# Performance work log

Hardware: AMD Instinct MI355X
Metric: run time of the kernel (lower is better)

## Reference

```python
import jax, jax.numpy as jnp
import numpy as np

B, S, D, H, DFF = 8, 1024, 1024, 16, 4096
DK = D // H
EPS = 1e-5


def setup_inputs() -> dict:
    key = jax.random.key(0)
    ks = jax.random.split(key, 12)
    sc = lambda n: 1.0 / np.sqrt(n)
    return {
        "x": jax.random.normal(ks[0], (B, S, D), jnp.float32),
        "src_mask": jnp.ones((B, 1, 1, S), jnp.int32),
        "wq": jax.random.normal(ks[1], (D, D), jnp.float32) * sc(D),
        "bq": jnp.zeros((D,), jnp.float32),
        "wk": jax.random.normal(ks[2], (D, D), jnp.float32) * sc(D),
        "bk": jnp.zeros((D,), jnp.float32),
        "wv": jax.random.normal(ks[3], (D, D), jnp.float32) * sc(D),
        "bv": jnp.zeros((D,), jnp.float32),
        "wo": jax.random.normal(ks[4], (D, D), jnp.float32) * sc(D),
        "bo": jnp.zeros((D,), jnp.float32),
        "w1": jax.random.normal(ks[5], (DFF, D), jnp.float32) * sc(D),
        "b1": jnp.zeros((DFF,), jnp.float32),
        "w2": jax.random.normal(ks[6], (D, DFF), jnp.float32) * sc(DFF),
        "b2": jnp.zeros((D,), jnp.float32),
        "g1": jnp.ones((1,), jnp.float32),
        "be1": jnp.zeros((1,), jnp.float32),
        "g2": jnp.ones((1,), jnp.float32),
        "be2": jnp.zeros((1,), jnp.float32),
    }


def _layernorm(x, gamma, beta):
    # Faithful to source: torch.var defaults to unbiased (ddof=1); scalar gamma/beta.
    mu = jnp.mean(x, axis=-1, keepdims=True)
    var = jnp.var(x, axis=-1, keepdims=True, ddof=1)
    return gamma * (x - mu) / jnp.sqrt(var + EPS) + beta


def _mha(x, wq, bq, wk, bk, wv, bv, wo, bo):
    q = (x @ wq.T + bq).reshape(B, S, H, DK).transpose(0, 2, 1, 3)
    k = (x @ wk.T + bk).reshape(B, S, H, DK).transpose(0, 2, 1, 3)
    v = (x @ wv.T + bv).reshape(B, S, H, DK).transpose(0, 2, 1, 3)
    scores = jnp.einsum("bhqd,bhkd->bhqk", q, k) / np.sqrt(DK)
    # NOTE: source uses non-inplace masked_fill whose result is discarded,
    # so the mask has no effect on the executed math; we replicate that.
    attn = jax.nn.softmax(scores, axis=-1)
    out = jnp.einsum("bhqk,bhkd->bhqd", attn, v)
    out = out.transpose(0, 2, 1, 3).reshape(B, S, D)
    return out @ wo.T + bo


def reference(x, src_mask, wq, bq, wk, bk, wv, bv, wo, bo,
              w1, b1, w2, b2, g1, be1, g2, be2):
    # residual 1: pre-norm self-attention (dropout=0 in eval)
    x = x + _mha(_layernorm(x, g1, be1), wq, bq, wk, bk, wv, bv, wo, bo)
    # residual 2: pre-norm FFN
    h = _layernorm(x, g2, be2)
    ff = jax.nn.relu(h @ w1.T + b1) @ w2.T + b2
    return x + ff
```

## Files before the change

kernel.cpp:

```cpp
#include <hip/hip_runtime.h>

typedef unsigned short u16;
typedef unsigned int u32;
typedef __attribute__((ext_vector_type(8))) __bf16 bf16x8;
typedef __attribute__((ext_vector_type(4))) float f32x4;

#define B_ 8
#define S_ 1024
#define D_ 1024
#define H_ 16
#define DK_ 64
#define DFF_ 4096
#define LDQKV 3072

__device__ __forceinline__ float bflo(u32 u) { return __uint_as_float(u << 16); }
__device__ __forceinline__ float bfhi(u32 u) { return __uint_as_float(u & 0xffff0000u); }
__device__ __forceinline__ u16 f2bf(float f) {
    u32 u = __float_as_uint(f);
    u += 0x7fffu + ((u >> 16) & 1u);
    return (u16)(u >> 16);
}
__device__ __forceinline__ u32 cvtpk(float lo, float hi) {
    u32 r;
    asm("v_cvt_pk_bf16_f32 %0, %1, %2" : "=v"(r) : "v"(lo), "v"(hi));
    return r;
}

__device__ __forceinline__ void gl2lds16(const u16* g, u16* l) {
    __builtin_amdgcn_global_load_lds(
        (const __attribute__((address_space(1))) void*)g,
        (__attribute__((address_space(3))) void*)l, 16, 0, 0);
}

__global__ __launch_bounds__(256) void sniff_kernel(const u16* __restrict__ w,
                                                    int* __restrict__ flag) {
    float mx = 0.f;
    for (int i = threadIdx.x; i < 4096; i += 256) {
        float v = fabsf(bflo((u32)w[i]));
        if (!isnan(v)) mx = fmaxf(mx, v);
    }
#pragma unroll
    for (int m = 1; m < 64; m <<= 1) mx = fmaxf(mx, __shfl_xor(mx, m, 64));
    __shared__ float wmx[4];
    if ((threadIdx.x & 63) == 0) wmx[threadIdx.x >> 6] = mx;
    __syncthreads();
    if (threadIdx.x == 0) {
        float m2 = fmaxf(fmaxf(wmx[0], wmx[1]), fmaxf(wmx[2], wmx[3]));
        *flag = (m2 > 1e3f) ? 1 : 0;
    }
}

__global__ __launch_bounds__(256) void norm_kernel(const void* __restrict__ in,
                                                   u16* __restrict__ out, int n,
                                                   const int* __restrict__ flag) {
    const int i = blockIdx.x * 256 + threadIdx.x;
    if (i >= n) return;
    if (*flag)
        out[i] = f2bf(((const float*)in)[i]);
    else
        out[i] = ((const u16*)in)[i];
}

struct SmallTbl {
    const void* src[10];
    u16* dst[10];
    int n[10];
};
__global__ __launch_bounds__(256) void norm_small(SmallTbl tb,
                                                  const int* __restrict__ flag) {
    int i = blockIdx.x * 256 + threadIdx.x;
    const int f = *flag;
#pragma unroll
    for (int j = 0; j < 10; ++j) {
        if (i < tb.n[j]) {
            if (f)
                tb.dst[j][i] = f2bf(((const float*)tb.src[j])[i]);
            else
                tb.dst[j][i] = ((const u16*)tb.src[j])[i];
            return;
        }
        i -= tb.n[j];
    }
}

template <int INF>
__global__ __launch_bounds__(256) void ln_kernel(const void* __restrict__ in,
                                                 const u16* __restrict__ gs,
                                                 const u16* __restrict__ bs,
                                                 u16* __restrict__ out,
                                                 const int* __restrict__ flag) {
    const int row = blockIdx.x, t = threadIdx.x;
    const bool f32in = (INF == 1) || (INF == 2 && flag[0] != 0);
    float v0, v1, v2, v3;
    if (f32in) {
        const float* p = (const float*)in + (size_t)row * D_ + t * 4;
        float4 f = *(const float4*)p;
        v0 = f.x; v1 = f.y; v2 = f.z; v3 = f.w;
    } else {
        const u16* p = (const u16*)in + (size_t)row * D_ + t * 4;
        uint2 u = *(const uint2*)p;
        v0 = bflo(u.x); v1 = bfhi(u.x); v2 = bflo(u.y); v3 = bfhi(u.y);
    }
    float s = v0 + v1 + v2 + v3;
    float sq = v0 * v0 + v1 * v1 + v2 * v2 + v3 * v3;
#pragma unroll
    for (int m = 1; m < 64; m <<= 1) {
        s += __shfl_xor(s, m, 64);
        sq += __shfl_xor(sq, m, 64);
    }
    __shared__ float ss[4], sqs[4];
    const int w = t >> 6;
    if ((t & 63) == 0) { ss[w] = s; sqs[w] = sq; }
    __syncthreads();
    s = ss[0] + ss[1] + ss[2] + ss[3];
    sq = sqs[0] + sqs[1] + sqs[2] + sqs[3];
    const float mu = s * (1.f / 1024.f);
    float var = (sq - 1024.f * mu * mu) * (1.f / 1023.f);
    var = fmaxf(var, 0.f);
    const float rstd = rsqrtf(var + 1e-5f);
    const float gm = bflo((u32)gs[0]);
    const float bt = bflo((u32)bs[0]);
    const float y0 = gm * (v0 - mu) * rstd + bt;
    const float y1 = gm * (v1 - mu) * rstd + bt;
    const float y2 = gm * (v2 - mu) * rstd + bt;
    const float y3 = gm * (v3 - mu) * rstd + bt;
    uint2 uo;
    uo.x = (u32)f2bf(y0) | ((u32)f2bf(y1) << 16);
    uo.y = (u32)f2bf(y2) | ((u32)f2bf(y3) << 16);
    *(uint2*)(out + (size_t)row * D_ + t * 4) = uo;
}

template <int RELU, int RES, int OUTF>
__global__ __launch_bounds__(256, 4) void gemm_bt(const u16* __restrict__ A,
                                                  const u16* __restrict__ W,
                                                  const u16* __restrict__ bias,
                                                  const void* __restrict__ res,
                                                  void* __restrict__ out,
                                                  int M, int N, int K,
                                                  const int* __restrict__ oflag) {
    __shared__ __align__(16) u16 As[128 * 64];
    __shared__ __align__(16) u16 Bs[128 * 64];
    const int t = threadIdx.x;
    const int lane = t & 63, w = t >> 6;
    const int wm = w >> 1, wn = w & 1;

    const int nx = N >> 7;
    const int gsz = nx << 3;
    const int id = blockIdx.x;
    const int grp = id / gsz;
    const int rem = id - grp * gsz;
    const int m0 = ((grp << 3) + (rem & 7)) << 7;
    const int n0 = (rem >> 3) << 7;

    f32x4 acc[4][4];
#pragma unroll
    for (int mi = 0; mi < 4; ++mi)
#pragma unroll
        for (int ni = 0; ni < 4; ++ni) acc[mi][ni] = (f32x4){0.f, 0.f, 0.f, 0.f};

    const int r8 = lane >> 3, s8 = lane & 7;
    const int cg = s8 ^ r8;
    const u16* Ag = A + (size_t)(m0 + w * 8 + r8) * K + cg * 8;
    const u16* Bg = W + (size_t)(n0 + w * 8 + r8) * K + cg * 8;
    const size_t rI = (size_t)32 * K;
    u16* Asd = &As[(w * 8) * 64];
    u16* Bsd = &Bs[(w * 8) * 64];

    const int c = lane & 15, g = lane >> 4;
    const u16* As_r = &As[(wm * 64 + c) * 64];
    const u16* Bs_r = &Bs[(wn * 64 + c) * 64];
    const int sl0 = (g ^ (c & 7)) * 8;
    const int sl1 = ((4 + g) ^ (c & 7)) * 8;

    for (int kt = 0; kt < K; kt += 64) {
        __syncthreads();
        gl2lds16(Ag, Asd);
        gl2lds16(Ag + rI, Asd + 32 * 64);
        gl2lds16(Ag + 2 * rI, Asd + 64 * 64);
        gl2lds16(Ag + 3 * rI, Asd + 96 * 64);
        gl2lds16(Bg, Bsd);
        gl2lds16(Bg + rI, Bsd + 32 * 64);
        gl2lds16(Bg + 2 * rI, Bsd + 64 * 64);
        gl2lds16(Bg + 3 * rI, Bsd + 96 * 64);
        Ag += 64; Bg += 64;
        __syncthreads();
#pragma unroll
        for (int kc = 0; kc < 2; ++kc) {
            const int sl = kc ? sl1 : sl0;
            bf16x8 af[4], bfr[4];
#pragma unroll
            for (int i = 0; i < 4; ++i) {
                af[i] = *(const bf16x8*)(As_r + i * 16 * 64 + sl);
                bfr[i] = *(const bf16x8*)(Bs_r + i * 16 * 64 + sl);
            }
#pragma unroll
            for (int mi = 0; mi < 4; ++mi)
#pragma unroll
                for (int ni = 0; ni < 4; ++ni)
                    acc[mi][ni] = __builtin_amdgcn_mfma_f32_16x16x32_bf16(af[mi], bfr[ni], acc[mi][ni], 0, 0, 0);
        }
    }

    const int fl = oflag ? oflag[0] : 0;
    const bool f32o = (OUTF == 1) || (OUTF == 2 && fl != 0);
    const int qd = lane >> 4, cl = lane & 15;
#pragma unroll
    for (int ni = 0; ni < 4; ++ni) {
        const int col = n0 + wn * 64 + ni * 16 + cl;
        const float bv = bflo((u32)bias[col]);
#pragma unroll
        for (int mi = 0; mi < 4; ++mi) {
#pragma unroll
            for (int j = 0; j < 4; ++j) {
                const int row = m0 + wm * 64 + mi * 16 + qd * 4 + j;
                float vv = acc[mi][ni][j] + bv;
                if (RELU) vv = fmaxf(vv, 0.f);
                if (RES == 2) vv += ((const float*)res)[(size_t)row * N + col];
                if (RES == 3) {
                    if (fl)
                        vv += ((const float*)res)[(size_t)row * N + col];
                    else
                        vv += bflo((u32)((const u16*)res)[(size_t)row * N + col]);
                }
                if (f32o)
                    ((float*)out)[(size_t)row * N + col] = vv;
                else
                    ((u16*)out)[(size_t)row * N + col] = f2bf(vv);
            }
        }
    }
}

template <int RELU>
__global__ __launch_bounds__(512, 2) void gemm256(const u16* __restrict__ A,
                                                  const u16* __restrict__ W,
                                                  const u16* __restrict__ bias,
                                                  u16* __restrict__ out,
                                                  int M, int N, int K) {
    __shared__ __align__(16) u16 As[2][2][256 * 32];
    __shared__ __align__(16) u16 Bs[2][2][256 * 32];
    const int t = threadIdx.x;
    const int lane = t & 63, w = t >> 6;
    const int wm = w >> 2, wn = w & 3;

    const int nx = N >> 8;
    const int gsz = nx << 3;
    const int id = blockIdx.x;
    const int grp = id / gsz;
    const int rem = id - grp * gsz;
    const int m0 = ((grp << 3) + (rem & 7)) << 8;
    const int n0 = (rem >> 3) << 8;

    f32x4 acc[8][4];
#pragma unroll
    for (int mi = 0; mi < 8; ++mi)
#pragma unroll
        for (int ni = 0; ni < 4; ++ni) acc[mi][ni] = (f32x4){0.f, 0.f, 0.f, 0.f};

    const int vr = lane >> 2, vs = lane & 3;
    const int cgs = vs ^ ((vr >> 1) & 3);
    const u16* Asrc = A + (size_t)(m0 + w * 16 + vr) * K + cgs * 8;
    const u16* Bsrc = W + (size_t)(n0 + w * 16 + vr) * K + cgs * 8;
    const size_t rI = (size_t)128 * K;

    auto stageA = [&](int p, int kc, int tk) {
        u16* d = &As[p][kc][(w * 16) * 32];
        const u16* s = Asrc + (size_t)tk * 64 + kc * 32;
        gl2lds16(s, d);
        gl2lds16(s + rI, d + 128 * 32);
    };
    auto stageB = [&](int p, int kc, int tk) {
        u16* d = &Bs[p][kc][(w * 16) * 32];
        const u16* s = Bsrc + (size_t)tk * 64 + kc * 32;
        gl2lds16(s, d);
        gl2lds16(s + rI, d + 128 * 32);
    };

    const int c = lane & 15, g = lane >> 4;
    const int sx = (g ^ ((c >> 1) & 3)) << 3;

    const int nt = K >> 6;
    stageA(0, 0, 0); stageB(0, 0, 0);
    stageA(0, 1, 0); stageB(0, 1, 0);
    stageA(1, 0, 1); stageB(1, 0, 1);
    asm volatile("s_waitcnt vmcnt(4)" ::: "memory");
    __builtin_amdgcn_s_barrier();
    __builtin_amdgcn_sched_barrier(0);

    int cur = 0;
    for (int kt = 0; kt < nt; ++kt) {
#pragma unroll
        for (int ph = 0; ph < 4; ++ph) {
            const int kc = ph >> 1, qm = ph & 1;
            bf16x8 af[4], bfv[4];
            const u16* Ab = &As[cur][kc][0];
            const u16* Bb = &Bs[cur][kc][0];
#pragma unroll
            for (int i = 0; i < 4; ++i)
                af[i] = *(const bf16x8*)(Ab + (wm * 128 + (qm * 4 + i) * 16 + c) * 32 + sx);
#pragma unroll
            for (int i = 0; i < 4; ++i)
                bfv[i] = *(const bf16x8*)(Bb + (wn * 64 + i * 16 + c) * 32 + sx);
            if (ph == 0) { if (kt + 1 < nt) stageA(cur ^ 1, 1, kt + 1); }
            else if (ph == 1) { if (kt + 1 < nt) stageB(cur ^ 1, 1, kt + 1); }
            else if (ph == 2) { if (kt + 2 < nt) stageA(cur, 0, kt + 2); }
            else { if (kt + 2 < nt) stageB(cur, 0, kt + 2); }
            __builtin_amdgcn_s_barrier();
            __builtin_amdgcn_s_setprio(1);
#pragma unroll
            for (int mi = 0; mi < 4; ++mi)
#pragma unroll
                for (int ni = 0; ni < 4; ++ni)
                    acc[qm * 4 + mi][ni] = __builtin_amdgcn_mfma_f32_16x16x32_bf16(
                        af[mi], bfv[ni], acc[qm * 4 + mi][ni], 0, 0, 0);
            __builtin_amdgcn_s_setprio(0);
            if (ph < 3) {
                __builtin_amdgcn_s_barrier();
                if (ph == 1) __builtin_amdgcn_sched_barrier(0);
            }
        }
        if (kt < nt - 2)
            asm volatile("s_waitcnt vmcnt(4)" ::: "memory");
        else
            asm volatile("s_waitcnt vmcnt(0)" ::: "memory");
        __builtin_amdgcn_s_barrier();
        __builtin_amdgcn_sched_barrier(0);
        cur ^= 1;
    }

#pragma unroll
    for (int mi = 0; mi < 8; ++mi) {
#pragma unroll
        for (int j = 0; j < 4; ++j) {
            const int row = m0 + wm * 128 + mi * 16 + g * 4 + j;
#pragma unroll
            for (int ni = 0; ni < 4; ++ni) {
                const int col = n0 + wn * 64 + ni * 16 + c;
                float vv = acc[mi][ni][j] + bflo((u32)bias[col]);
                if (RELU) vv = fmaxf(vv, 0.f);
                out[(size_t)row * N + col] = f2bf(vv);
            }
        }
    }
}

__global__ __launch_bounds__(256, 2) void attn_mfma(const u16* __restrict__ QKV,
                                                    u16* __restrict__ O) {
    __shared__ __align__(16) u16 lds[6 * 64 * 64];
    u16* Ks = lds;
    u16* VsT = lds + 64 * 64;

    const int t = threadIdx.x;
    const int lane = t & 63, w = t >> 6;
    u16* Pw = lds + (2 + w) * 64 * 64;
    const int b = blockIdx.y >> 4, h = blockIdx.y & 15;
    const int q_base = blockIdx.x * 256 + w * 64;
    const int c = lane & 15, g = lane >> 4;
    const int c7 = c & 7;
    const float SC = 0.18033688011112042f;

    bf16x8 qfrag[4][2];
#pragma unroll
    for (int ni = 0; ni < 4; ++ni)
#pragma unroll
        for (int kc = 0; kc < 2; ++kc)
            qfrag[ni][kc] = *(const bf16x8*)(QKV + (size_t)(b * S_ + q_base + 16 * ni + c) * LDQKV +
                                             h * 64 + kc * 32 + 8 * g);

    f32x4 acc_o[4][4];
#pragma unroll
    for (int mi = 0; mi < 4; ++mi)
#pragma unroll
        for (int ni = 0; ni < 4; ++ni) acc_o[mi][ni] = (f32x4){0.f, 0.f, 0.f, 0.f};
    float m_st[4] = {-1e30f, -1e30f, -1e30f, -1e30f};
    float l_st[4] = {0.f, 0.f, 0.f, 0.f};

    const size_t kbase = (size_t)(b * S_) * LDQKV + 1024 + h * 64;
    const size_t vbase = (size_t)(b * S_) * LDQKV + 2048 + h * 64;

    const int r8 = lane >> 3, s8 = lane & 7;
    const int cgk = s8 ^ r8;
    const u16* Kg = QKV + kbase + (size_t)(w * 8 + r8) * LDQKV + cgk * 8;
    u16* Ksd = &Ks[(w * 8) * 64];
    const size_t rIk = (size_t)32 * LDQKV;

    const int vr = t >> 3, vdq = t & 7;
    const u16* Vg = QKV + vbase + (size_t)(2 * vr) * LDQKV + vdq * 8;

    int vfx[4];
#pragma unroll
    for (int mi = 0; mi < 4; ++mi) vfx[mi] = c7 ^ ((2 * mi + (c >> 3)) & 7);

    for (int kt = 0; kt < 16; ++kt) {
        __syncthreads();
        gl2lds16(Kg, Ksd);
        gl2lds16(Kg + rIk, Ksd + 32 * 64);
        Kg += (size_t)64 * LDQKV;
        {
            uint4 a = *(const uint4*)Vg;
            uint4 bb = *(const uint4*)(Vg + LDQKV);
            Vg += (size_t)64 * LDQKV;
            const u32 aw[4] = {a.x, a.y, a.z, a.w};
            const u32 bw[4] = {bb.x, bb.y, bb.z, bb.w};
#pragma unroll
            for (int i = 0; i < 8; ++i) {
                u32 wv;
                if (i & 1)
                    wv = (aw[i >> 1] >> 16) | (bw[i >> 1] & 0xffff0000u);
                else
                    wv = (aw[i >> 1] & 0xffffu) | (bw[i >> 1] << 16);
                const int d = vdq * 8 + i;
                *(u32*)&VsT[d * 64 + (((vr >> 2) ^ (i ^ vdq)) << 3) + ((vr & 3) << 1)] = wv;
            }
        }
        __syncthreads();

        f32x4 acc_s[4][4];
#pragma unroll
        for (int mi = 0; mi < 4; ++mi)
#pragma unroll
            for (int ni = 0; ni < 4; ++ni) acc_s[mi][ni] = (f32x4){0.f, 0.f, 0.f, 0.f};
        __builtin_amdgcn_s_setprio(1);
#pragma unroll
        for (int kc = 0; kc < 2; ++kc) {
            bf16x8 kf[4];
#pragma unroll
            for (int mi = 0; mi < 4; ++mi)
                kf[mi] = *(const bf16x8*)&Ks[(16 * mi + c) * 64 + (((kc * 4 + g) ^ c7) << 3)];
#pragma unroll
            for (int mi = 0; mi < 4; ++mi)
#pragma unroll
                for (int ni = 0; ni < 4; ++ni)
                    acc_s[mi][ni] = __builtin_amdgcn_mfma_f32_16x16x32_bf16(
                        kf[mi], qfrag[ni][kc], acc_s[mi][ni], 0, 0, 0);
        }
        __builtin_amdgcn_s_setprio(0);

        float alpha[4];
        bool resc[4];
#pragma unroll
        for (int ni = 0; ni < 4; ++ni) {
            float mx = -1e30f;
#pragma unroll
            for (int mi = 0; mi < 4; ++mi) {
#pragma unroll
                for (int j = 0; j < 4; ++j) mx = fmaxf(mx, acc_s[mi][ni][j]);
            }
            mx = fmaxf(mx, __shfl_xor(mx, 16, 64));
            mx = fmaxf(mx, __shfl_xor(mx, 32, 64));
            const float mo = m_st[ni];
            const float mn = fmaxf(mo, mx);
            resc[ni] = __any(mn > mo);
            if (resc[ni]) {
                alpha[ni] = exp2f((mo - mn) * SC);
                m_st[ni] = mn;
            } else {
                alpha[ni] = 1.f;
            }
            const float nms = m_st[ni] * SC;
            float sum = 0.f;
#pragma unroll
            for (int mi = 0; mi < 4; ++mi) {
                const float p0 = exp2f(fmaf(acc_s[mi][ni][0], SC, -nms));
                const float p1 = exp2f(fmaf(acc_s[mi][ni][1], SC, -nms));
                const float p2 = exp2f(fmaf(acc_s[mi][ni][2], SC, -nms));
                const float p3 = exp2f(fmaf(acc_s[mi][ni][3], SC, -nms));
                sum += (p0 + p1) + (p2 + p3);
                uint2 pk;
                pk.x = cvtpk(p0, p1);
                pk.y = cvtpk(p2, p3);
                *(uint2*)&Pw[(16 * ni + c) * 64 +
                             ((((2 * mi + (g >> 1)) ^ c7) << 3) + ((g & 1) << 2))] = pk;
            }
            sum += __shfl_xor(sum, 16, 64);
            sum += __shfl_xor(sum, 32, 64);
            l_st[ni] = (resc[ni] ? l_st[ni] * alpha[ni] : l_st[ni]) + sum;
        }
#pragma unroll
        for (int ni = 0; ni < 4; ++ni) {
            if (resc[ni]) {
#pragma unroll
                for (int mi = 0; mi < 4; ++mi) {
#pragma unroll
                    for (int j = 0; j < 4; ++j) acc_o[mi][ni][j] *= alpha[ni];
                }
            }
        }

        __builtin_amdgcn_s_setprio(1);
#pragma unroll
        for (int kc = 0; kc < 2; ++kc) {
            bf16x8 vf[4], pf[4];
#pragma unroll
            for (int mi = 0; mi < 4; ++mi)
                vf[mi] = *(const bf16x8*)&VsT[(16 * mi + c) * 64 + (((kc * 4 + g) ^ vfx[mi]) << 3)];
#pragma unroll
            for (int ni = 0; ni < 4; ++ni)
                pf[ni] = *(const bf16x8*)&Pw[(16 * ni + c) * 64 + (((kc * 4 + g) ^ c7) << 3)];
#pragma unroll
            for (int mi = 0; mi < 4; ++mi)
#pragma unroll
                for (int ni = 0; ni < 4; ++ni)
                    acc_o[mi][ni] = __builtin_amdgcn_mfma_f32_16x16x32_bf16(
                        vf[mi], pf[ni], acc_o[mi][ni], 0, 0, 0);
        }
        __builtin_amdgcn_s_setprio(0);
    }

#pragma unroll
    for (int ni = 0; ni < 4; ++ni) {
        const float inv_l = 1.f / l_st[ni];
        u16* op = O + (size_t)(b * S_ + q_base + 16 * ni + c) * D_ + h * 64;
#pragma unroll
        for (int mi = 0; mi < 4; ++mi) {
            uint2 uo;
            uo.x = cvtpk(acc_o[mi][ni][0] * inv_l, acc_o[mi][ni][1] * inv_l);
            uo.y = cvtpk(acc_o[mi][ni][2] * inv_l, acc_o[mi][ni][3] * inv_l);
            *(uint2*)(op + 16 * mi + 4 * g) = uo;
        }
    }
}

extern "C" void kernel_launch(void* const* d_in, const int* in_sizes, int n_in,
                              void* d_out, int out_size, void* d_ws, size_t ws_size,
                              hipStream_t stream) {
    (void)in_sizes; (void)n_in; (void)out_size; (void)ws_size;
    char* ws = (char*)d_ws;
    const size_t MB = 1ull << 20;
    const size_t KB = 1024;
    u16* wqkv = (u16*)(ws + 16 * MB);
    u16* won  = (u16*)(ws + 22 * MB);
    u16* w1n  = (u16*)(ws + 24 * MB);
    u16* w2n  = (u16*)(ws + 32 * MB);
    u16* bqkv = (u16*)(ws + 40 * MB);
    u16* bon  = (u16*)(ws + 40 * MB + 64 * KB);
    u16* b1n  = (u16*)(ws + 40 * MB + 128 * KB);
    u16* b2n  = (u16*)(ws + 40 * MB + 192 * KB);
    u16* g1n  = (u16*)(ws + 40 * MB + 256 * KB);
    u16* be1n = (u16*)(ws + 40 * MB + 320 * KB);
    u16* g2n  = (u16*)(ws + 40 * MB + 384 * KB);
    u16* be2n = (u16*)(ws + 40 * MB + 448 * KB);
    int* flag = (int*)(ws + 40 * MB + 512 * KB);
    u16* h1   = (u16*)(ws + 48 * MB);
    u16* qkv  = (u16*)(ws + 64 * MB);
    float* x2 = (float*)(ws + 64 * MB);
    u16* h2   = (u16*)(ws + 96 * MB);
    u16* f1   = (u16*)(ws + 112 * MB);

    const int M = B_ * S_;

    sniff_kernel<<<1, 256, 0, stream>>>((const u16*)d_in[2], flag);
    auto nrm = [&](const void* in, u16* out, int n) {
        norm_kernel<<<(n + 255) / 256, 256, 0, stream>>>(in, out, n, flag);
    };
    nrm(d_in[2],  wqkv,               D_ * D_);
    nrm(d_in[4],  wqkv + D_ * D_,     D_ * D_);
    nrm(d_in[6],  wqkv + 2 * D_ * D_, D_ * D_);
    nrm(d_in[8],  won, D_ * D_);
    nrm(d_in[10], w1n, DFF_ * D_);
    nrm(d_in[12], w2n, D_ * DFF_);
    {
        SmallTbl tb;
        tb.src[0] = d_in[3];  tb.dst[0] = bqkv;          tb.n[0] = D_;
        tb.src[1] = d_in[5];  tb.dst[1] = bqkv + D_;     tb.n[1] = D_;
        tb.src[2] = d_in[7];  tb.dst[2] = bqkv + 2 * D_; tb.n[2] = D_;
        tb.src[3] = d_in[9];  tb.dst[3] = bon;           tb.n[3] = D_;
        tb.src[4] = d_in[11]; tb.dst[4] = b1n;           tb.n[4] = DFF_;
        tb.src[5] = d_in[13]; tb.dst[5] = b2n;           tb.n[5] = D_;
        tb.src[6] = d_in[14]; tb.dst[6] = g1n;           tb.n[6] = 1;
        tb.src[7] = d_in[15]; tb.dst[7] = be1n;          tb.n[7] = 1;
        tb.src[8] = d_in[16]; tb.dst[8] = g2n;           tb.n[8] = 1;
        tb.src[9] = d_in[17]; tb.dst[9] = be2n;          tb.n[9] = 1;
        const int tot = 5 * D_ + DFF_ + 4;
        norm_small<<<(tot + 255) / 256, 256, 0, stream>>>(tb, flag);
    }

    ln_kernel<2><<<M, 256, 0, stream>>>(d_in[0], g1n, be1n, h1, flag);
    gemm256<0><<<(LDQKV / 256) * (M / 256), 512, 0, stream>>>(h1, wqkv, bqkv, qkv, M, LDQKV, D_);
    attn_mfma<<<dim3(S_ / 256, B_ * H_), 256, 0, stream>>>(qkv, h1);
    gemm_bt<0, 3, 1><<<(D_ / 128) * (M / 128), 256, 0, stream>>>(h1, won, bon, d_in[0], x2, M, D_, D_, flag);
    ln_kernel<1><<<M, 256, 0, stream>>>((const void*)x2, g2n, be2n, h2, flag);
    gemm256<1><<<(DFF_ / 256) * (M / 256), 512, 0, stream>>>(h2, w1n, b1n, f1, M, DFF_, D_);
    gemm_bt<0, 2, 2><<<(D_ / 128) * (M / 128), 256, 0, stream>>>(f1, w2n, b2n, (const void*)x2, (void*)d_out, M, D_, DFF_, flag);
}
```

Baseline: 531.4 us.

## Add 128x256 eight-wave GEMM for output projection and FFN down-projection

Adds gemm_bn, a 512-thread GEMM with a 128x256 output tile, double-buffered direct global-to-LDS staging split across four phases, and swizzled LDS reads. It replaces the 128x128 gemm_bt kernels used for the attention output projection and the FFN second layer, with grouped block ordering for L2 reuse. The larger tile raises arithmetic intensity per block and overlaps loads with MFMA. The trade-off is half as many blocks for N=1024, which may reduce occupancy or balance across CUs.

```diff
diff --git a/kernel.cpp b/kernel.cpp
--- a/kernel.cpp
+++ b/kernel.cpp
@@ -339,6 +339,131 @@
                 float vv = acc[mi][ni][j] + bflo((u32)bias[col]);
                 if (RELU) vv = fmaxf(vv, 0.f);
                 out[(size_t)row * N + col] = f2bf(vv);
+            }
+        }
+    }
+}
+
+template <int RELU, int RES, int OUTF>
+__global__ __launch_bounds__(512, 2) void gemm_bn(const u16* __restrict__ A,
+                                                  const u16* __restrict__ W,
+                                                  const u16* __restrict__ bias,
+                                                  const void* __restrict__ res,
+                                                  void* __restrict__ out,
+                                                  int M, int N, int K,
+                                                  const int* __restrict__ oflag) {
+    __shared__ __align__(16) u16 As[2][2][128 * 32];
+    __shared__ __align__(16) u16 Bs[2][2][256 * 32];
+    const int t = threadIdx.x;
+    const int lane = t & 63, w = t >> 6;
+    const int wm = w >> 2, wn = w & 3;
+
+    const int nx = N >> 8;
+    const int gsz = nx << 3;
+    const int id = blockIdx.x;
+    const int grp = id / gsz;
+    const int rem = id - grp * gsz;
+    const int m0 = ((grp << 3) + (rem & 7)) << 7;
+    const int n0 = (rem >> 3) << 8;
+
+    f32x4 acc[4][4];
+#pragma unroll
+    for (int mi = 0; mi < 4; ++mi)
+#pragma unroll
+        for (int ni = 0; ni < 4; ++ni) acc[mi][ni] = (f32x4){0.f, 0.f, 0.f, 0.f};
+
+    const int vr = lane >> 2, vs = lane & 3;
+    const int cgs = vs ^ ((vr >> 1) & 3);
+    const u16* Asrc = A + (size_t)(m0 + w * 16 + vr) * K + cgs * 8;
+    const u16* Bsrc = W + (size_t)(n0 + w * 16 + vr) * K + cgs * 8;
+    const size_t rI = (size_t)128 * K;
+
+    auto stageA = [&](int p, int kc, int tk) {
+        u16* d = &As[p][kc][(w * 16) * 32];
+        gl2lds16(Asrc + (size_t)tk * 64 + kc * 32, d);
+    };
+    auto stageB = [&](int p, int kc, int tk) {
+        u16* d = &Bs[p][kc][(w * 16) * 32];
+        const u16* s = Bsrc + (size_t)tk * 64 + kc * 32;
+        gl2lds16(s, d);
+        gl2lds16(s + rI, d + 128 * 32);
+    };
+
+    const int c = lane & 15, g = lane >> 4;
+    const int sx = (g ^ ((c >> 1) & 3)) << 3;
+
+    const int nt = K >> 6;
+    stageA(0, 0, 0); stageB(0, 0, 0);
+    stageA(0, 1, 0); stageB(0, 1, 0);
+    stageA(1, 0, 1); stageB(1, 0, 1);
+    asm volatile("s_waitcnt vmcnt(3)" ::: "memory");
+    __builtin_amdgcn_s_barrier();
+    __builtin_amdgcn_sched_barrier(0);
+
+    int cur = 0;
+    for (int kt = 0; kt < nt; ++kt) {
+#pragma unroll
+        for (int ph = 0; ph < 4; ++ph) {
+            const int kc = ph >> 1, qm = ph & 1;
+            bf16x8 af[2], bfv[4];
+            const u16* Ab = &As[cur][kc][0];
+            const u16* Bb = &Bs[cur][kc][0];
+#pragma unroll
+            for (int i = 0; i < 2; ++i)
+                af[i] = *(const bf16x8*)(Ab + (wm * 64 + (qm * 2 + i) * 16 + c) * 32 + sx);
+#pragma unroll
+            for (int i = 0; i < 4; ++i)
+                bfv[i] = *(const bf16x8*)(Bb + (wn * 64 + i * 16 + c) * 32 + sx);
+            if (ph == 0) { if (kt + 1 < nt) stageA(cur ^ 1, 1, kt + 1); }
+            else if (ph == 1) { if (kt + 1 < nt) stageB(cur ^ 1, 1, kt + 1); }
+            else if (ph == 2) { if (kt + 2 < nt) stageA(cur, 0, kt + 2); }
+            else { if (kt + 2 < nt) stageB(cur, 0, kt + 2); }
+            __builtin_amdgcn_s_barrier();
+            __builtin_amdgcn_s_setprio(1);
+#pragma unroll
+            for (int mi = 0; mi < 2; ++mi)
+#pragma unroll
+                for (int ni = 0; ni < 4; ++ni)
+                    acc[qm * 2 + mi][ni] = __builtin_amdgcn_mfma_f32_16x16x32_bf16(
+                        af[mi], bfv[ni], acc[qm * 2 + mi][ni], 0, 0, 0);
+            __builtin_amdgcn_s_setprio(0);
+            if (ph < 3) {
+                __builtin_amdgcn_s_barrier();
+                if (ph == 1) __builtin_amdgcn_sched_barrier(0);
+            }
+        }
+        if (kt < nt - 2)
+            asm volatile("s_waitcnt vmcnt(3)" ::: "memory");
+        else
+            asm volatile("s_waitcnt vmcnt(0)" ::: "memory");
+        __builtin_amdgcn_s_barrier();
+        __builtin_amdgcn_sched_barrier(0);
+        cur ^= 1;
+    }
+
+    const int fl = oflag ? oflag[0] : 0;
+    const bool f32o = (OUTF == 1) || (OUTF == 2 && fl != 0);
+#pragma unroll
+    for (int mi = 0; mi < 4; ++mi) {
+#pragma unroll
+        for (int j = 0; j < 4; ++j) {
+            const int row = m0 + wm * 64 + mi * 16 + g * 4 + j;
+#pragma unroll
+            for (int ni = 0; ni < 4; ++ni) {
+                const int col = n0 + wn * 64 + ni * 16 + c;
+                float vv = acc[mi][ni][j] + bflo((u32)bias[col]);
+                if (RELU) vv = fmaxf(vv, 0.f);
+                if (RES == 2) vv += ((const float*)res)[(size_t)row * N + col];
+                if (RES == 3) {
+                    if (fl)
+                        vv += ((const float*)res)[(size_t)row * N + col];
+                    else
+                        vv += bflo((u32)((const u16*)res)[(size_t)row * N + col]);
+                }
+                if (f32o)
+                    ((float*)out)[(size_t)row * N + col] = vv;
+                else
+                    ((u16*)out)[(size_t)row * N + col] = f2bf(vv);
             }
         }
     }
@@ -578,8 +703,8 @@
     ln_kernel<2><<<M, 256, 0, stream>>>(d_in[0], g1n, be1n, h1, flag);
     gemm256<0><<<(LDQKV / 256) * (M / 256), 512, 0, stream>>>(h1, wqkv, bqkv, qkv, M, LDQKV, D_);
     attn_mfma<<<dim3(S_ / 256, B_ * H_), 256, 0, stream>>>(qkv, h1);
-    gemm_bt<0, 3, 1><<<(D_ / 128) * (M / 128), 256, 0, stream>>>(h1, won, bon, d_in[0], x2, M, D_, D_, flag);
+    gemm_bn<0, 3, 1><<<(M / 128) * (D_ / 256), 512, 0, stream>>>(h1, won, bon, d_in[0], x2, M, D_, D_, flag);
     ln_kernel<1><<<M, 256, 0, stream>>>((const void*)x2, g2n, be2n, h2, flag);
     gemm256<1><<<(DFF_ / 256) * (M / 256), 512, 0, stream>>>(h2, w1n, b1n, f1, M, DFF_, D_);
-    gemm_bt<0, 2, 2><<<(D_ / 128) * (M / 128), 256, 0, stream>>>(f1, w2n, b2n, (const void*)x2, (void*)d_out, M, D_, DFF_, flag);
-}
+    gemm_bn<0, 2, 2><<<(M / 128) * (D_ / 256), 512, 0, stream>>>(f1, w2n, b2n, (const void*)x2, (void*)d_out, M, D_, DFF_, flag);
+}
```

New measurement: 556.3 us. +4.7%, slower.

## Replace N=1024 GEMMs with pipelined 128x256 tile kernel using async LDS staging

Applied to the files above, without the earlier changes.

The output-projection and FFN-down GEMMs (N=1024) move from a simple 128x128 single-buffered kernel to a new 512-thread kernel with 128x256 tiles. It reuses the double-buffered, split-K-chunk global-to-LDS pipeline and barrier/priority scheduling of the gemm256 kernel. The goal is to hide load latency behind MFMA work and raise data reuse per block. The cost is halving the grid to 256 blocks, which is roughly one wave on the device and may leave CUs underused, especially for the K=1024 projection.

```diff
diff --git a/kernel.cpp b/kernel.cpp
--- a/kernel.cpp
+++ b/kernel.cpp
@@ -130,27 +130,140 @@
     *(uint2*)(out + (size_t)row * D_ + t * 4) = uo;
 }
 
+template <int RELU>
+__global__ __launch_bounds__(512, 2) void gemm256(const u16* __restrict__ A,
+                                                  const u16* __restrict__ W,
+                                                  const u16* __restrict__ bias,
+                                                  u16* __restrict__ out,
+                                                  int M, int N, int K) {
+    __shared__ __align__(16) u16 As[2][2][256 * 32];
+    __shared__ __align__(16) u16 Bs[2][2][256 * 32];
+    const int t = threadIdx.x;
+    const int lane = t & 63, w = t >> 6;
+    const int wm = w >> 2, wn = w & 3;
+
+    const int nx = N >> 8;
+    const int gsz = nx << 3;
+    const int id = blockIdx.x;
+    const int grp = id / gsz;
+    const int rem = id - grp * gsz;
+    const int m0 = ((grp << 3) + (rem & 7)) << 8;
+    const int n0 = (rem >> 3) << 8;
+
+    f32x4 acc[8][4];
+#pragma unroll
+    for (int mi = 0; mi < 8; ++mi)
+#pragma unroll
+        for (int ni = 0; ni < 4; ++ni) acc[mi][ni] = (f32x4){0.f, 0.f, 0.f, 0.f};
+
+    const int vr = lane >> 2, vs = lane & 3;
+    const int cgs = vs ^ ((vr >> 1) & 3);
+    const u16* Asrc = A + (size_t)(m0 + w * 16 + vr) * K + cgs * 8;
+    const u16* Bsrc = W + (size_t)(n0 + w * 16 + vr) * K + cgs * 8;
+    const size_t rI = (size_t)128 * K;
+
+    auto stageA = [&](int p, int kc, int tk) {
+        u16* d = &As[p][kc][(w * 16) * 32];
+        const u16* s = Asrc + (size_t)tk * 64 + kc * 32;
+        gl2lds16(s, d);
+        gl2lds16(s + rI, d + 128 * 32);
+    };
+    auto stageB = [&](int p, int kc, int tk) {
+        u16* d = &Bs[p][kc][(w * 16) * 32];
+        const u16* s = Bsrc + (size_t)tk * 64 + kc * 32;
+        gl2lds16(s, d);
+        gl2lds16(s + rI, d + 128 * 32);
+    };
+
+    const int c = lane & 15, g = lane >> 4;
+    const int sx = (g ^ ((c >> 1) & 3)) << 3;
+
+    const int nt = K >> 6;
+    stageA(0, 0, 0); stageB(0, 0, 0);
+    stageA(0, 1, 0); stageB(0, 1, 0);
+    stageA(1, 0, 1); stageB(1, 0, 1);
+    asm volatile("s_waitcnt vmcnt(4)" ::: "memory");
+    __builtin_amdgcn_s_barrier();
+    __builtin_amdgcn_sched_barrier(0);
+
+    int cur = 0;
+    for (int kt = 0; kt < nt; ++kt) {
+#pragma unroll
+        for (int ph = 0; ph < 4; ++ph) {
+            const int kc = ph >> 1, qm = ph & 1;
+            bf16x8 af[4], bfv[4];
+            const u16* Ab = &As[cur][kc][0];
+            const u16* Bb = &Bs[cur][kc][0];
+#pragma unroll
+            for (int i = 0; i < 4; ++i)
+                af[i] = *(const bf16x8*)(Ab + (wm * 128 + (qm * 4 + i) * 16 + c) * 32 + sx);
+#pragma unroll
+            for (int i = 0; i < 4; ++i)
+                bfv[i] = *(const bf16x8*)(Bb + (wn * 64 + i * 16 + c) * 32 + sx);
+            if (ph == 0) { if (kt + 1 < nt) stageA(cur ^ 1, 1, kt + 1); }
+            else if (ph == 1) { if (kt + 1 < nt) stageB(cur ^ 1, 1, kt + 1); }
+            else if (ph == 2) { if (kt + 2 < nt) stageA(cur, 0, kt + 2); }
+            else { if (kt + 2 < nt) stageB(cur, 0, kt + 2); }
+            __builtin_amdgcn_s_barrier();
+            __builtin_amdgcn_s_setprio(1);
+#pragma unroll
+            for (int mi = 0; mi < 4; ++mi)
+#pragma unroll
+                for (int ni = 0; ni < 4; ++ni)
+                    acc[qm * 4 + mi][ni] = __builtin_amdgcn_mfma_f32_16x16x32_bf16(
+                        af[mi], bfv[ni], acc[qm * 4 + mi][ni], 0, 0, 0);
+            __builtin_amdgcn_s_setprio(0);
+            if (ph < 3) {
+                __builtin_amdgcn_s_barrier();
+                if (ph == 1) __builtin_amdgcn_sched_barrier(0);
+            }
+        }
+        if (kt < nt - 2)
+            asm volatile("s_waitcnt vmcnt(4)" ::: "memory");
+        else
+            asm volatile("s_waitcnt vmcnt(0)" ::: "memory");
+        __builtin_amdgcn_s_barrier();
+        __builtin_amdgcn_sched_barrier(0);
+        cur ^= 1;
+    }
+
+#pragma unroll
+    for (int mi = 0; mi < 8; ++mi) {
+#pragma unroll
+        for (int j = 0; j < 4; ++j) {
+            const int row = m0 + wm * 128 + mi * 16 + g * 4 + j;
+#pragma unroll
+            for (int ni = 0; ni < 4; ++ni) {
+                const int col = n0 + wn * 64 + ni * 16 + c;
+                float vv = acc[mi][ni][j] + bflo((u32)bias[col]);
+                if (RELU) vv = fmaxf(vv, 0.f);
+                out[(size_t)row * N + col] = f2bf(vv);
+            }
+        }
+    }
+}
+
 template <int RELU, int RES, int OUTF>
-__global__ __launch_bounds__(256, 4) void gemm_bt(const u16* __restrict__ A,
+__global__ __launch_bounds__(512, 2) void gemm_bn(const u16* __restrict__ A,
                                                   const u16* __restrict__ W,
                                                   const u16* __restrict__ bias,
                                                   const void* __restrict__ res,
                                                   void* __restrict__ out,
                                                   int M, int N, int K,
                                                   const int* __restrict__ oflag) {
-    __shared__ __align__(16) u16 As[128 * 64];
-    __shared__ __align__(16) u16 Bs[128 * 64];
+    __shared__ __align__(16) u16 As[2][2][128 * 32];
+    __shared__ __align__(16) u16 Bs[2][2][256 * 32];
     const int t = threadIdx.x;
     const int lane = t & 63, w = t >> 6;
-    const int wm = w >> 1, wn = w & 1;
-
-    const int nx = N >> 7;
+    const int wm = w >> 2, wn = w & 3;
+
+    const int nx = N >> 8;
     const int gsz = nx << 3;
     const int id = blockIdx.x;
     const int grp = id / gsz;
     const int rem = id - grp * gsz;
     const int m0 = ((grp << 3) + (rem & 7)) << 7;
-    const int n0 = (rem >> 3) << 7;
+    const int n0 = (rem >> 3) << 8;
 
     f32x4 acc[4][4];
 #pragma unroll
@@ -158,62 +271,100 @@
 #pragma unroll
         for (int ni = 0; ni < 4; ++ni) acc[mi][ni] = (f32x4){0.f, 0.f, 0.f, 0.f};
 
-    const int r8 = lane >> 3, s8 = lane & 7;
-    const int cg = s8 ^ r8;
-    const u16* Ag = A + (size_t)(m0 + w * 8 + r8) * K + cg * 8;
-    const u16* Bg = W + (size_t)(n0 + w * 8 + r8) * K + cg * 8;
-    const size_t rI = (size_t)32 * K;
-    u16* Asd = &As[(w * 8) * 64];
-    u16* Bsd = &Bs[(w * 8) * 64];
+    const int vr = lane >> 2, vs = lane & 3;
+    const int cgs = vs ^ ((vr >> 1) & 3);
+    const u16* Asrc = A + (size_t)(m0 + w * 16 + vr) * K + cgs * 8;
+    const u16* Bsrc = W + (size_t)(n0 + w * 16 + vr) * K + cgs * 8;
+    const size_t rI = (size_t)128 * K;
+
+    auto stageA = [&](int p, int kc, int tk) {
+        u16* d = &As[p][kc][(w * 16) * 32];
+        gl2lds16(Asrc + (size_t)tk * 64 + kc * 32, d);
+    };
+    auto stageB = [&](int p, int kc, int tk) {
+        u16* d = &Bs[p][kc][(w * 16) * 32];
+        const u16* s = Bsrc + (size_t)tk * 64 + kc * 32;
+        gl2lds16(s, d);
+        gl2lds16(s + rI, d + 128 * 32);
+    };
 
     const int c = lane & 15, g = lane >> 4;
-    const u16* As_r = &As[(wm * 64 + c) * 64];
-    const u16* Bs_r = &Bs[(wn * 64 + c) * 64];
-    const int sl0 = (g ^ (c & 7)) * 8;
-    const int sl1 = ((4 + g) ^ (c & 7)) * 8;
-
-    for (int kt = 0; kt < K; kt += 64) {
-        __syncthreads();
-        gl2lds16(Ag, Asd);
-        gl2lds16(Ag + rI, Asd + 32 * 64);
-        gl2lds16(Ag + 2 * rI, Asd + 64 * 64);
-        gl2lds16(Ag + 3 * rI, Asd + 96 * 64);
-        gl2lds16(Bg, Bsd);
-        gl2lds16(Bg + rI, Bsd + 32 * 64);
-        gl2lds16(Bg + 2 * rI, Bsd + 64 * 64);
-        gl2lds16(Bg + 3 * rI, Bsd + 96 * 64);
-        Ag += 64; Bg += 64;
-        __syncthreads();
-#pragma unroll
-        for (int kc = 0; kc < 2; ++kc) {
-            const int sl = kc ? sl1 : sl0;
-            bf16x8 af[4], bfr[4];
-#pragma unroll
-            for (int i = 0; i < 4; ++i) {
-                af[i] = *(const bf16x8*)(As_r + i * 16 * 64 + sl);
-                bfr[i] = *(const bf16x8*)(Bs_r + i * 16 * 64 + sl);
-            }
+    const int sx = (g ^ ((c >> 1) & 3)) << 3;
+
+    const int nt = K >> 6;
+    stageA(0, 0, 0); stageB(0, 0, 0);
+    stageA(0, 1, 0); stageB(0, 1, 0);
+    stageA(1, 0, 1); stageB(1, 0, 1);
+    asm volatile("s_waitcnt vmcnt(3)" ::: "memory");
+    __builtin_amdgcn_s_barrier();
+    __builtin_amdgcn_sched_barrier(0);
+
+    int cur = 0;
+    for (int kt = 0; kt < nt; ++kt) {
+        {
+            bf16x8 af[4], bfv[4];
+            const u16* Ab = &As[cur][0][0];
+            const u16* Bb = &Bs[cur][0][0];
+#pragma unroll
+            for (int i = 0; i < 4; ++i)
+                af[i] = *(const bf16x8*)(Ab + (wm * 64 + i * 16 + c) * 32 + sx);
+#pragma unroll
+            for (int i = 0; i < 4; ++i)
+                bfv[i] = *(const bf16x8*)(Bb + (wn * 64 + i * 16 + c) * 32 + sx);
+            if (kt + 1 < nt) { stageA(cur ^ 1, 1, kt + 1); stageB(cur ^ 1, 1, kt + 1); }
+            __builtin_amdgcn_s_barrier();
+            __builtin_amdgcn_s_setprio(1);
 #pragma unroll
             for (int mi = 0; mi < 4; ++mi)
 #pragma unroll
                 for (int ni = 0; ni < 4; ++ni)
-                    acc[mi][ni] = __builtin_amdgcn_mfma_f32_16x16x32_bf16(af[mi], bfr[ni], acc[mi][ni], 0, 0, 0);
-        }
+                    acc[mi][ni] = __builtin_amdgcn_mfma_f32_16x16x32_bf16(
+                        af[mi], bfv[ni], acc[mi][ni], 0, 0, 0);
+            __builtin_amdgcn_s_setprio(0);
+            __builtin_amdgcn_s_barrier();
+            __builtin_amdgcn_sched_barrier(0);
+        }
+        {
+            bf16x8 af[4], bfv[4];
+            const u16* Ab = &As[cur][1][0];
+            const u16* Bb = &Bs[cur][1][0];
+#pragma unroll
+            for (int i = 0; i < 4; ++i)
+                af[i] = *(const bf16x8*)(Ab + (wm * 64 + i * 16 + c) * 32 + sx);
+#pragma unroll
+            for (int i = 0; i < 4; ++i)
+                bfv[i] = *(const bf16x8*)(Bb + (wn * 64 + i * 16 + c) * 32 + sx);
+            if (kt + 2 < nt) { stageA(cur, 0, kt + 2); stageB(cur, 0, kt + 2); }
+            __builtin_amdgcn_s_barrier();
+            __builtin_amdgcn_s_setprio(1);
+#pragma unroll
+            for (int mi = 0; mi < 4; ++mi)
+#pragma unroll
+                for (int ni = 0; ni < 4; ++ni)
+                    acc[mi][ni] = __builtin_amdgcn_mfma_f32_16x16x32_bf16(
+                        af[mi], bfv[ni], acc[mi][ni], 0, 0, 0);
+            __builtin_amdgcn_s_setprio(0);
+        }
+        if (kt < nt - 2)
+            asm volatile("s_waitcnt vmcnt(3)" ::: "memory");
+        else
+            asm volatile("s_waitcnt vmcnt(0)" ::: "memory");
+        __builtin_amdgcn_s_barrier();
+        __builtin_amdgcn_sched_barrier(0);
+        cur ^= 1;
     }
 
     const int fl = oflag ? oflag[0] : 0;
     const bool f32o = (OUTF == 1) || (OUTF == 2 && fl != 0);
-    const int qd = lane >> 4, cl = lane & 15;
-#pragma unroll
-    for (int ni = 0; ni < 4; ++ni) {
-        const int col = n0 + wn * 64 + ni * 16 + cl;
-        const float bv = bflo((u32)bias[col]);
-#pragma unroll
-        for (int mi = 0; mi < 4; ++mi) {
-#pragma unroll
-            for (int j = 0; j < 4; ++j) {
-                const int row = m0 + wm * 64 + mi * 16 + qd * 4 + j;
-                float vv = acc[mi][ni][j] + bv;
+#pragma unroll
+    for (int mi = 0; mi < 4; ++mi) {
+#pragma unroll
+        for (int j = 0; j < 4; ++j) {
+            const int row = m0 + wm * 64 + mi * 16 + g * 4 + j;
+#pragma unroll
+            for (int ni = 0; ni < 4; ++ni) {
+                const int col = n0 + wn * 64 + ni * 16 + c;
+                float vv = acc[mi][ni][j] + bflo((u32)bias[col]);
                 if (RELU) vv = fmaxf(vv, 0.f);
                 if (RES == 2) vv += ((const float*)res)[(size_t)row * N + col];
                 if (RES == 3) {
@@ -226,119 +377,6 @@
                     ((float*)out)[(size_t)row * N + col] = vv;
                 else
                     ((u16*)out)[(size_t)row * N + col] = f2bf(vv);
-            }
-        }
-    }
-}
-
-template <int RELU>
-__global__ __launch_bounds__(512, 2) void gemm256(const u16* __restrict__ A,
-                                                  const u16* __restrict__ W,
-                                                  const u16* __restrict__ bias,
-                                                  u16* __restrict__ out,
-                                                  int M, int N, int K) {
-    __shared__ __align__(16) u16 As[2][2][256 * 32];
-    __shared__ __align__(16) u16 Bs[2][2][256 * 32];
-    const int t = threadIdx.x;
-    const int lane = t & 63, w = t >> 6;
-    const int wm = w >> 2, wn = w & 3;
-
-    const int nx = N >> 8;
-    const int gsz = nx << 3;
-    const int id = blockIdx.x;
-    const int grp = id / gsz;
-    const int rem = id - grp * gsz;
-    const int m0 = ((grp << 3) + (rem & 7)) << 8;
-    const int n0 = (rem >> 3) << 8;
-
-    f32x4 acc[8][4];
-#pragma unroll
-    for (int mi = 0; mi < 8; ++mi)
-#pragma unroll
-        for (int ni = 0; ni < 4; ++ni) acc[mi][ni] = (f32x4){0.f, 0.f, 0.f, 0.f};
-
-    const int vr = lane >> 2, vs = lane & 3;
-    const int cgs = vs ^ ((vr >> 1) & 3);
-    const u16* Asrc = A + (size_t)(m0 + w * 16 + vr) * K + cgs * 8;
-    const u16* Bsrc = W + (size_t)(n0 + w * 16 + vr) * K + cgs * 8;
-    const size_t rI = (size_t)128 * K;
-
-    auto stageA = [&](int p, int kc, int tk) {
-        u16* d = &As[p][kc][(w * 16) * 32];
-        const u16* s = Asrc + (size_t)tk * 64 + kc * 32;
-        gl2lds16(s, d);
-        gl2lds16(s + rI, d + 128 * 32);
-    };
-    auto stageB = [&](int p, int kc, int tk) {
-        u16* d = &Bs[p][kc][(w * 16) * 32];
-        const u16* s = Bsrc + (size_t)tk * 64 + kc * 32;
-        gl2lds16(s, d);
-        gl2lds16(s + rI, d + 128 * 32);
-    };
-
-    const int c = lane & 15, g = lane >> 4;
-    const int sx = (g ^ ((c >> 1) & 3)) << 3;
-
-    const int nt = K >> 6;
-    stageA(0, 0, 0); stageB(0, 0, 0);
-    stageA(0, 1, 0); stageB(0, 1, 0);
-    stageA(1, 0, 1); stageB(1, 0, 1);
-    asm volatile("s_waitcnt vmcnt(4)" ::: "memory");
-    __builtin_amdgcn_s_barrier();
-    __builtin_amdgcn_sched_barrier(0);
-
-    int cur = 0;
-    for (int kt = 0; kt < nt; ++kt) {
-#pragma unroll
-        for (int ph = 0; ph < 4; ++ph) {
-            const int kc = ph >> 1, qm = ph & 1;
-            bf16x8 af[4], bfv[4];
-            const u16* Ab = &As[cur][kc][0];
-            const u16* Bb = &Bs[cur][kc][0];
-#pragma unroll
-            for (int i = 0; i < 4; ++i)
-                af[i] = *(const bf16x8*)(Ab + (wm * 128 + (qm * 4 + i) * 16 + c) * 32 + sx);
-#pragma unroll
-            for (int i = 0; i < 4; ++i)
-                bfv[i] = *(const bf16x8*)(Bb + (wn * 64 + i * 16 + c) * 32 + sx);
-            if (ph == 0) { if (kt + 1 < nt) stageA(cur ^ 1, 1, kt + 1); }
-            else if (ph == 1) { if (kt + 1 < nt) stageB(cur ^ 1, 1, kt + 1); }
-            else if (ph == 2) { if (kt + 2 < nt) stageA(cur, 0, kt + 2); }
-            else { if (kt + 2 < nt) stageB(cur, 0, kt + 2); }
-            __builtin_amdgcn_s_barrier();
-            __builtin_amdgcn_s_setprio(1);
-#pragma unroll
-            for (int mi = 0; mi < 4; ++mi)
-#pragma unroll
-                for (int ni = 0; ni < 4; ++ni)
-                    acc[qm * 4 + mi][ni] = __builtin_amdgcn_mfma_f32_16x16x32_bf16(
-                        af[mi], bfv[ni], acc[qm * 4 + mi][ni], 0, 0, 0);
-            __builtin_amdgcn_s_setprio(0);
-            if (ph < 3) {
-                __builtin_amdgcn_s_barrier();
-                if (ph == 1) __builtin_amdgcn_sched_barrier(0);
-            }
-        }
-        if (kt < nt - 2)
-            asm volatile("s_waitcnt vmcnt(4)" ::: "memory");
-        else
-            asm volatile("s_waitcnt vmcnt(0)" ::: "memory");
-        __builtin_amdgcn_s_barrier();
-        __builtin_amdgcn_sched_barrier(0);
-        cur ^= 1;
-    }
-
-#pragma unroll
-    for (int mi = 0; mi < 8; ++mi) {
-#pragma unroll
-        for (int j = 0; j < 4; ++j) {
-            const int row = m0 + wm * 128 + mi * 16 + g * 4 + j;
-#pragma unroll
-            for (int ni = 0; ni < 4; ++ni) {
-                const int col = n0 + wn * 64 + ni * 16 + c;
-                float vv = acc[mi][ni][j] + bflo((u32)bias[col]);
-                if (RELU) vv = fmaxf(vv, 0.f);
-                out[(size_t)row * N + col] = f2bf(vv);
             }
         }
     }
@@ -578,8 +616,8 @@
     ln_kernel<2><<<M, 256, 0, stream>>>(d_in[0], g1n, be1n, h1, flag);
     gemm256<0><<<(LDQKV / 256) * (M / 256), 512, 0, stream>>>(h1, wqkv, bqkv, qkv, M, LDQKV, D_);
     attn_mfma<<<dim3(S_ / 256, B_ * H_), 256, 0, stream>>>(qkv, h1);
-    gemm_bt<0, 3, 1><<<(D_ / 128) * (M / 128), 256, 0, stream>>>(h1, won, bon, d_in[0], x2, M, D_, D_, flag);
+    gemm_bn<0, 3, 1><<<(M / 128) * (D_ / 256), 512, 0, stream>>>(h1, won, bon, d_in[0], x2, M, D_, D_, flag);
     ln_kernel<1><<<M, 256, 0, stream>>>((const void*)x2, g2n, be2n, h2, flag);
     gemm256<1><<<(DFF_ / 256) * (M / 256), 512, 0, stream>>>(h2, w1n, b1n, f1, M, DFF_, D_);
-    gemm_bt<0, 2, 2><<<(D_ / 128) * (M / 128), 256, 0, stream>>>(f1, w2n, b2n, (const void*)x2, (void*)d_out, M, D_, DFF_, flag);
-}
+    gemm_bn<0, 2, 2><<<(M / 128) * (D_ / 256), 512, 0, stream>>>(f1, w2n, b2n, (const void*)x2, (void*)d_out, M, D_, DFF_, flag);
+}
```

Result: no change. 539.5 us (+1.5%).
